# Kernel optimization log

Measured on AMD Instinct MI355X. Metric: run time of the kernel, lower is better.

## Reference

```python
import jax, jax.numpy as jnp
import numpy as np

B, C, H, W = 8, 512, 64, 64
HID = 4 * C  # MixFFN hidden = in_dim*4
FOCUS = 3.0


def _ln(x, g, b, eps=1e-5):
    m = x.mean(-1, keepdims=True)
    v = ((x - m) ** 2).mean(-1, keepdims=True)
    return (x - m) / jnp.sqrt(v + eps) * g + b


def setup_inputs() -> dict:
    key = jax.random.key(0)
    ks = jax.random.split(key, 12)
    init = lambda k, shape, fan: (jax.random.normal(k, shape, jnp.float32) / np.float32(np.sqrt(fan)))
    d = {}
    d['x'] = jax.random.normal(ks[0], (B, C, H, W), jnp.float32)
    # 1x1 conv weights stored as (Cout, Cin)
    d['Wq'] = init(ks[1], (C, C), C); d['bq'] = jnp.zeros((C,), jnp.float32)
    d['Wk'] = init(ks[2], (C, C), C); d['bk'] = jnp.zeros((C,), jnp.float32)
    d['Wv'] = init(ks[3], (C, C), C); d['bv'] = jnp.zeros((C,), jnp.float32)
    d['scale'] = jnp.zeros((1, 1, C), jnp.float32)  # nn.Parameter(torch.zeros)
    # MixFFN_skip params
    d['fc1_w'] = init(ks[4], (C, HID), C); d['fc1_b'] = jnp.zeros((HID,), jnp.float32)
    d['dw_w'] = init(ks[5], (HID, 1, 3, 3), 9); d['dw_b'] = jnp.zeros((HID,), jnp.float32)
    d['fc2_w'] = init(ks[6], (HID, C), HID); d['fc2_b'] = jnp.zeros((C,), jnp.float32)
    d['ln1_g'] = jnp.ones((HID,), jnp.float32); d['ln1_b'] = jnp.zeros((HID,), jnp.float32)
    d['lnm_g'] = jnp.ones((C,), jnp.float32); d['lnm_b'] = jnp.zeros((C,), jnp.float32)
    return d


def _forward(x, Wq, bq, Wk, bk, Wv, bv, scale, fc1_w, fc1_b, dw_w, dw_b, fc2_w, fc2_b, ln1_g, ln1_b, lnm_g, lnm_b):
    b, c, h, w = x.shape
    n = h * w
    # 1x1 convs (NCHW), then RAW reshape to (B, N, C) as in torch (no permute!)
    conv1 = lambda t, Wm, bm: jnp.einsum('bchw,oc->bohw', t, Wm) + bm[None, :, None, None]
    q = jax.nn.softmax(conv1(x, Wq, bq).reshape(b, n, c), axis=1)
    k = jax.nn.softmax(conv1(x, Wk, bk).reshape(b, n, c), axis=2)
    v = conv1(x, Wv, bv).reshape(b, n, c)
    q = jax.nn.relu(q) + 1e-6
    k = jax.nn.relu(k) + 1e-6
    sc = jax.nn.softplus(scale)
    q = q / sc
    k = k / sc
    q_norm = jnp.linalg.norm(q, axis=-1, keepdims=True)
    k_norm = jnp.linalg.norm(k, axis=-1, keepdims=True)
    q = q ** FOCUS  # focusing_factor <= 6 branch
    k = k ** FOCUS
    q = q / jnp.linalg.norm(q, axis=-1, keepdims=True) * q_norm
    k = k / jnp.linalg.norm(k, axis=-1, keepdims=True) * k_norm
    # num_heads == 1: (b h) n c == b n c
    z = 1.0 / (jnp.einsum('bic,bc->bi', q, k.sum(axis=1)) + 1e-6)
    kv = jnp.einsum('bjc,bjd->bcd', k, v)  # O(N) linear attention summary
    attn = jnp.einsum('bic,bcd,bi->bid', q, kv, z)
    shortcut = jnp.transpose(x, (0, 2, 3, 1)).reshape(b, n, c)  # proper rearrange b c h w -> b (h w) c
    enhanced = shortcut + attn
    # MixFFN_skip(norm_mlp(enhanced), h, w)
    t = _ln(enhanced, lnm_g, lnm_b)
    a = t @ fc1_w + fc1_b  # (B, N, HID)
    ai = jnp.transpose(a, (0, 2, 1)).reshape(b, HID, h, w)
    dw = jax.lax.conv_general_dilated(ai, dw_w, (1, 1), 'SAME',
                                      dimension_numbers=('NCHW', 'OIHW', 'NCHW'),
                                      feature_group_count=HID)
    dw = dw + dw_b[None, :, None, None]
    dw = jnp.transpose(dw.reshape(b, HID, n), (0, 2, 1))
    ax = jax.nn.gelu(_ln(dw + a, ln1_g, ln1_b), approximate=False)
    mlp_out = ax @ fc2_w + fc2_b
    out = enhanced + mlp_out
    return out.reshape(b, h, w, c)


def reference(x, Wq, bq, Wk, bk, Wv, bv, scale, fc1_w, fc1_b, dw_w, dw_b, fc2_w, fc2_b, ln1_g, ln1_b, lnm_g, lnm_b):
    return _forward(x, Wq, bq, Wk, bk, Wv, bv, scale, fc1_w, fc1_b, dw_w, dw_b, fc2_w, fc2_b, ln1_g, ln1_b, lnm_g, lnm_b)
```

## Files before the change

### kernel.cpp

```cpp
#include <hip/hip_runtime.h>
#include <hip/hip_bf16.h>

typedef __hip_bfloat16 bf16;
typedef __attribute__((ext_vector_type(8))) short bh8;
typedef __attribute__((ext_vector_type(4))) short bh4;
typedef __attribute__((ext_vector_type(4))) float f32x4;

#define CDIM 512
#define NDIM 4096
#define HIDD 2048
#define BATCH 8

__device__ __forceinline__ float bf2f(short s) {
    union { unsigned u; float f; } c; c.u = ((unsigned)(unsigned short)s) << 16; return c.f;
}
__device__ __forceinline__ short f2bf(float f) {
    union { __hip_bfloat16 h; short s; } c; c.h = __float2bfloat16(f); return c.s;
}
__device__ __forceinline__ float wsum(float v) {
#pragma unroll
    for (int o = 32; o; o >>= 1) v += __shfl_xor(v, o);
    return v;
}
__device__ __forceinline__ float wmax(float v) {
#pragma unroll
    for (int o = 32; o; o >>= 1) v = fmaxf(v, __shfl_xor(v, o));
    return v;
}

#define GLL(g, l) __builtin_amdgcn_global_load_lds( \
    (const __attribute__((address_space(1))) unsigned int*)(g), \
    (__attribute__((address_space(3))) unsigned int*)(l), 16, 0, 0)

enum { EP_QEXP = 0, EP_BF16_BROW = 1, EP_ATTN = 3, EP_BF16_BCOL = 4, EP_OUT = 5, EP_QKV = 6 };

template<int MODE, int TM, int MFAST>
__global__ __launch_bounds__(256)
void gemm_bt(const bf16* __restrict__ A, int lda, long sA,
             const bf16* __restrict__ Bt, int ldb, long sB,
             void* __restrict__ Cp, int ldc, long sC, int K,
             const float* __restrict__ bias,
             const void* __restrict__ aux1, long sAux1,
             const void* __restrict__ aux2, long sAux2)
{
    constexpr int MF = TM / 32;
    __shared__ __align__(16) bf16 As[TM * 64];
    __shared__ __align__(16) bf16 Bs[128 * 64];
    int bx, by, bz;
    {
        const int gx = gridDim.x, gy = gridDim.y;
        const int nwg = gx * gy * gridDim.z;
        int lid = blockIdx.x + gx * (blockIdx.y + gy * blockIdx.z);
        const int cpx = nwg >> 3;
        int swz = (lid & 7) * cpx + (lid >> 3);
        if constexpr (MFAST) {
            by = swz % gy; swz /= gy;
            bx = swz % gx;
            bz = swz / gx;
        } else {
            bx = swz % gx; swz /= gx;
            by = swz % gy;
            bz = swz / gy;
        }
    }
    const bf16* Ab = A + (long)bz * sA + (long)by * TM * lda;
    const bf16* Bb = Bt + (long)bz * sB + (long)bx * 128 * ldb;
    const int t = threadIdx.x, lane = t & 63, wid = t >> 6;
    const int wm = wid >> 1, wn = wid & 1, lg = lane >> 4, lr = lane & 15;

    f32x4 acc[MF][4];
#pragma unroll
    for (int m = 0; m < MF; ++m)
#pragma unroll
        for (int n = 0; n < 4; ++n) acc[m][n] = (f32x4){0.f, 0.f, 0.f, 0.f};

    for (int kt = 0; kt < K; kt += 64) {
#pragma unroll
        for (int i = 0; i < MF; ++i) {
            const int ch = i * 256 + t;
            const int row = ch >> 3;
            const int cs = (ch & 7) ^ (row & 7);
            GLL(Ab + (long)row * lda + kt + (cs << 3), (char*)As + i * 4096 + wid * 1024);
        }
#pragma unroll
        for (int i = 0; i < 4; ++i) {
            const int ch = i * 256 + t;
            const int row = ch >> 3;
            const int cs = (ch & 7) ^ (row & 7);
            GLL(Bb + (long)row * ldb + kt + (cs << 3), (char*)Bs + i * 4096 + wid * 1024);
        }
        __syncthreads();
#pragma unroll
        for (int kk = 0; kk < 2; ++kk) {
            bh8 af[MF], bfv[4];
#pragma unroll
            for (int m = 0; m < MF; ++m) {
                const int row = wm * (TM / 2) + m * 16 + lr;
                const int kc = (kk * 4 + lg) ^ (row & 7);
                af[m] = *(const bh8*)(As + row * 64 + kc * 8);
            }
#pragma unroll
            for (int n = 0; n < 4; ++n) {
                const int row = wn * 64 + n * 16 + lr;
                const int kc = (kk * 4 + lg) ^ (row & 7);
                bfv[n] = *(const bh8*)(Bs + row * 64 + kc * 8);
            }
#pragma unroll
            for (int m = 0; m < MF; ++m)
#pragma unroll
                for (int n = 0; n < 4; ++n)
                    acc[m][n] = __builtin_amdgcn_mfma_f32_16x16x32_bf16(af[m], bfv[n], acc[m][n], 0, 0, 0);
        }
        __syncthreads();
    }

    const int gr0 = by * TM + wm * (TM / 2);
    const int gc0 = bx * 128 + wn * 64;
#pragma unroll
    for (int m = 0; m < MF; ++m) {
#pragma unroll
        for (int n = 0; n < 4; ++n) {
            const int gc = gc0 + n * 16 + lr;
#pragma unroll
            for (int r = 0; r < 4; ++r) {
                const int gr = gr0 + m * 16 + lg * 4 + r;
                float v = acc[m][n][r];
                if constexpr (MODE == EP_QKV) {
                    const int which = gr >> 9, grl = gr & 511;
                    const float vb_ = v + bias[gr];
                    if (which == 0)
                        ((bf16*)Cp + (long)bz * sC)[(long)grl * ldc + gc] = __float2bfloat16(expf(vb_));
                    else if (which == 1)
                        ((bf16*)aux1 + (long)bz * sC)[(long)grl * ldc + gc] = __float2bfloat16(vb_);
                    else
                        ((bf16*)aux2 + (long)bz * sC)[(long)grl * ldc + gc] = __float2bfloat16(vb_);
                } else if constexpr (MODE == EP_QEXP) {
                    ((bf16*)Cp + (long)bz * sC)[(long)gr * ldc + gc] = __float2bfloat16(expf(v + bias[gr]));
                } else if constexpr (MODE == EP_BF16_BROW) {
                    ((bf16*)Cp + (long)bz * sC)[(long)gr * ldc + gc] = __float2bfloat16(v + bias[gr]);
                } else if constexpr (MODE == EP_ATTN) {
                    const bf16* xg = (const bf16*)aux1 + (long)bz * sAux1;
                    const float* zg = (const float*)aux2 + (long)bz * sAux2;
                    ((float*)Cp + (long)bz * sC)[(long)gr * ldc + gc] =
                        zg[gr] * v + bf2f(*(const short*)(xg + (long)gr * 512 + gc));
                } else if constexpr (MODE == EP_BF16_BCOL) {
                    ((bf16*)Cp + (long)bz * sC)[(long)gr * ldc + gc] = __float2bfloat16(v + bias[gc]);
                } else {
                    float* op = (float*)Cp;
                    const long idx = (long)gr * ldc + gc;
                    op[idx] = v + bias[gc] + ((const float*)aux1)[idx];
                }
            }
        }
    }
}

__global__ __launch_bounds__(256)
void gemm_tn_splitk(const bf16* __restrict__ A, int lda, long sA,
                    const bf16* __restrict__ B, int ldb, long sB,
                    bf16* __restrict__ part)
{
    __shared__ __align__(16) short As[64 * 128];
    __shared__ __align__(16) short Bs[64 * 128];
    int bx, by, bzl;
    {
        const int gx = gridDim.x, gy = gridDim.y;
        const int nwg = gx * gy * gridDim.z;
        int lid = blockIdx.x + gx * (blockIdx.y + gy * blockIdx.z);
        const int cpx = nwg >> 3;
        int swz = (lid & 7) * cpx + (lid >> 3);
        bx = swz % gx; swz /= gx;
        by = swz % gy;
        bzl = swz / gy;
    }
    const int bz = bzl >> 2, ks = bzl & 3;
    const bf16* Ab = A + (long)bz * sA + (long)ks * 1024 * lda + by * 128;
    const bf16* Bb = B + (long)bz * sB + (long)ks * 1024 * ldb + bx * 128;
    const int t = threadIdx.x, lane = t & 63, wid = t >> 6;
    const int wm = wid >> 1, wn = wid & 1, lg = lane >> 4, lr = lane & 15;

    f32x4 acc[4][4];
#pragma unroll
    for (int m = 0; m < 4; ++m)
#pragma unroll
        for (int n = 0; n < 4; ++n) acc[m][n] = (f32x4){0.f, 0.f, 0.f, 0.f};

    for (int kt = 0; kt < 1024; kt += 64) {
#pragma unroll
        for (int i = 0; i < 4; ++i) {
            const int ch = i * 256 + t;
            const int row = ch >> 4;
            const int cs = (ch & 15) ^ (((row >> 3) & 3) << 1);
            GLL(Ab + (long)(kt + row) * lda + (cs << 3), (char*)As + i * 4096 + wid * 1024);
            GLL(Bb + (long)(kt + row) * ldb + (cs << 3), (char*)Bs + i * 4096 + wid * 1024);
        }
        __syncthreads();
#pragma unroll
        for (int kk = 0; kk < 2; ++kk) {
            bh8 af[4], bfv[4];
#pragma unroll
            for (int m = 0; m < 4; ++m) {
                const int col = wm * 64 + m * 16 + lr;
#pragma unroll
                for (int u = 0; u < 8; ++u) {
                    const int row = kk * 32 + lg * 8 + u;
                    af[m][u] = As[row * 128 + (((col >> 3) ^ (((row >> 3) & 3) << 1)) << 3) + (col & 7)];
                }
            }
#pragma unroll
            for (int n = 0; n < 4; ++n) {
                const int col = wn * 64 + n * 16 + lr;
#pragma unroll
                for (int u = 0; u < 8; ++u) {
                    const int row = kk * 32 + lg * 8 + u;
                    bfv[n][u] = Bs[row * 128 + (((col >> 3) ^ (((row >> 3) & 3) << 1)) << 3) + (col & 7)];
                }
            }
#pragma unroll
            for (int m = 0; m < 4; ++m)
#pragma unroll
                for (int n = 0; n < 4; ++n)
                    acc[m][n] = __builtin_amdgcn_mfma_f32_16x16x32_bf16(af[m], bfv[n], acc[m][n], 0, 0, 0);
        }
        __syncthreads();
    }

    bf16* po = part + ((long)bzl << 18);
    const int gr0 = by * 128 + wm * 64;
    const int gc0 = bx * 128 + wn * 64;
#pragma unroll
    for (int m = 0; m < 4; ++m)
#pragma unroll
        for (int n = 0; n < 4; ++n) {
            const int gc = gc0 + n * 16 + lr;
#pragma unroll
            for (int r = 0; r < 4; ++r) {
                const int gr = gr0 + m * 16 + lg * 4 + r;
                po[(long)gr * 512 + gc] = __float2bfloat16(acc[m][n][r]);
            }
        }
}

__global__ __launch_bounds__(256)
void k_kvred(const bf16* __restrict__ part, bf16* __restrict__ kvt)
{
    const long e = ((long)blockIdx.x * 256 + threadIdx.x) * 8;
    const int b = (int)(e >> 18);
    const int off = (int)(e & 262143);
    float s[8] = {0.f, 0.f, 0.f, 0.f, 0.f, 0.f, 0.f, 0.f};
#pragma unroll
    for (int ks = 0; ks < 4; ++ks) {
        bh8 v = *(const bh8*)(part + (((long)(b * 4 + ks)) << 18) + off);
#pragma unroll
        for (int j = 0; j < 8; ++j) s[j] += bf2f(v[j]);
    }
    bh8 o;
#pragma unroll
    for (int j = 0; j < 8; ++j) o[j] = f2bf(s[j]);
    *(bh8*)(kvt + ((long)b << 18) + off) = o;
}

__global__ __launch_bounds__(256)
void k_transpose(const float* __restrict__ src, bf16* __restrict__ dst,
                 int Rd, int Cd, long sSrc, long sDst)
{
    __shared__ float tile[64][65];
    const float* s = src + (long)blockIdx.z * sSrc;
    bf16* d = dst + (long)blockIdx.z * sDst;
    const int r0 = blockIdx.x * 64, c0 = blockIdx.y * 64;
    const int t = threadIdx.x;
#pragma unroll 4
    for (int i = 0; i < 16; ++i) {
        int idx = i * 256 + t;
        int a = idx >> 6, b = idx & 63;
        tile[a][b] = s[(long)(c0 + a) * Rd + r0 + b];
    }
    __syncthreads();
#pragma unroll 4
    for (int i = 0; i < 16; ++i) {
        int idx = i * 256 + t;
        int a = idx >> 6, b = idx & 63;
        d[(long)(r0 + a) * Cd + c0 + b] = __float2bfloat16(tile[b][a]);
    }
}

__global__ void k_setup(const float* __restrict__ Wq, const float* __restrict__ Wk,
                        const float* __restrict__ Wv, bf16* __restrict__ oq,
                        bf16* __restrict__ ok, bf16* __restrict__ ov,
                        const float* __restrict__ scale, float* __restrict__ invsc,
                        const float* __restrict__ w, float* __restrict__ wT,
                        const float* __restrict__ bq, const float* __restrict__ bk,
                        const float* __restrict__ bv, float* __restrict__ bqkv) {
    int i = blockIdx.x * 256 + threadIdx.x;
    if (i < 262144) {
        oq[i] = __float2bfloat16(Wq[i]);
        ok[i] = __float2bfloat16(Wk[i]);
        ov[i] = __float2bfloat16(Wv[i]);
    }
    if (i < 512) invsc[i] = 1.0f / log1pf(expf(scale[i]));
    if (i < 1536) bqkv[i] = (i < 512 ? bq[i] : (i < 1024 ? bk[i - 512] : bv[i - 1024]));
    if (i < HIDD * 9) {
        int chn = i / 9, kk = i % 9;
        wT[kk * HIDD + chn] = w[i];
    }
}

__global__ void k_fill(float* o, int n, float v) {
    int i = blockIdx.x * 256 + threadIdx.x; if (i < n) o[i] = v;
}

__global__ __launch_bounds__(256)
void k_colsums(const bf16* __restrict__ qe, const bf16* __restrict__ kb,
               float* __restrict__ qpart, float* __restrict__ kpart) {
    const int xb = blockIdx.x;
    const int ic = blockIdx.y, b = blockIdx.z;
    const int j = (xb & 1) * 256 + threadIdx.x;
    const bf16* src = (xb < 2) ? qe : kb;
    const bf16* p = src + (long)b * (NDIM * CDIM) + (long)ic * 256 * CDIM + j;
    float s = 0.f;
    for (int i = 0; i < 256; ++i) s += bf2f(*(const short*)(p + (long)i * CDIM));
    ((xb < 2) ? qpart : kpart)[((long)b * 16 + ic) * CDIM + j] = s;
}

__global__ __launch_bounds__(256)
void k_red2(const float* __restrict__ qpart, float* __restrict__ qsum,
            const float* __restrict__ kpart, float* __restrict__ ksum) {
    const int idx = blockIdx.x * 256 + threadIdx.x;
    const int which = idx >> 12, r = idx & 4095;
    const int b = r >> 9, c = r & 511;
    const float* src = which ? kpart : qpart;
    float s = 0.f;
#pragma unroll
    for (int jc = 0; jc < 16; ++jc) s += src[((long)(b * 16 + jc)) * CDIM + c];
    (which ? ksum : qsum)[r] = s;
}

__global__ __launch_bounds__(256)
void k_qrow(const bf16* __restrict__ qe, const float* __restrict__ qsum,
            const float* __restrict__ invsc, bf16* __restrict__ qb,
            const float* __restrict__ ksum, float* __restrict__ z)
{
    const long row = (long)blockIdx.x * 4 + (threadIdx.x >> 6);
    const int lane = threadIdx.x & 63;
    const int b = (int)(row >> 12);
    bh8 ev = *(const bh8*)(qe + row * CDIM + lane * 8);
    const float* qs = qsum + b * CDIM + lane * 8;
    const float* is = invsc + lane * 8;
    f32x4 s0 = *(const f32x4*)qs, s1 = *(const f32x4*)(qs + 4);
    f32x4 i0 = *(const f32x4*)is, i1 = *(const f32x4*)(is + 4);
    float q[8];
#pragma unroll
    for (int k = 0; k < 4; ++k) {
        q[k]     = (bf2f(ev[k]) / s0[k] + 1e-6f) * i0[k];
        q[k + 4] = (bf2f(ev[k + 4]) / s1[k] + 1e-6f) * i1[k];
    }
    float s2 = 0.f, s6 = 0.f, q3[8];
#pragma unroll
    for (int k = 0; k < 8; ++k) { s2 += q[k] * q[k]; float c = q[k] * q[k] * q[k]; q3[k] = c; s6 += c * c; }
    s2 = wsum(s2); s6 = wsum(s6);
    const float sc = sqrtf(s2) / sqrtf(s6);
    bh8 o;
#pragma unroll
    for (int k = 0; k < 8; ++k) o[k] = f2bf(q3[k] * sc);
    *(bh8*)(qb + row * CDIM + lane * 8) = o;
    const float* ks = ksum + (long)b * CDIM + lane * 8;
    f32x4 k0 = *(const f32x4*)ks, k1 = *(const f32x4*)(ks + 4);
    float zd = 0.f;
#pragma unroll
    for (int j = 0; j < 4; ++j) { zd += bf2f(o[j]) * k0[j]; zd += bf2f(o[j + 4]) * k1[j]; }
    zd = wsum(zd);
    if (lane == 0) z[row] = 1.0f / (zd + 1e-6f);
}

__global__ __launch_bounds__(256)
void k_krow(bf16* __restrict__ kb, const float* __restrict__ invsc)
{
    const long row = (long)blockIdx.x * 4 + (threadIdx.x >> 6);
    const int lane = threadIdx.x & 63;
    bh8 v = *(const bh8*)(kb + row * CDIM + lane * 8);
    const float* is = invsc + lane * 8;
    f32x4 i0 = *(const f32x4*)is, i1 = *(const f32x4*)(is + 4);
    float xv[8];
#pragma unroll
    for (int k = 0; k < 8; ++k) xv[k] = bf2f(v[k]);
    float mx = -1e30f;
#pragma unroll
    for (int k = 0; k < 8; ++k) mx = fmaxf(mx, xv[k]);
    mx = wmax(mx);
    float e[8], se = 0.f;
#pragma unroll
    for (int k = 0; k < 8; ++k) { e[k] = expf(xv[k] - mx); se += e[k]; }
    se = wsum(se);
    const float inv = 1.0f / se;
    float q[8];
#pragma unroll
    for (int k = 0; k < 4; ++k) {
        q[k]     = (e[k] * inv + 1e-6f) * i0[k];
        q[k + 4] = (e[k + 4] * inv + 1e-6f) * i1[k];
    }
    float s2 = 0.f, s6 = 0.f, q3[8];
#pragma unroll
    for (int k = 0; k < 8; ++k) { s2 += q[k] * q[k]; float c = q[k] * q[k] * q[k]; q3[k] = c; s6 += c * c; }
    s2 = wsum(s2); s6 = wsum(s6);
    const float sc = sqrtf(s2) / sqrtf(s6);
    bh8 o;
#pragma unroll
    for (int k = 0; k < 8; ++k) o[k] = f2bf(q3[k] * sc);
    *(bh8*)(kb + row * CDIM + lane * 8) = o;
}

__global__ __launch_bounds__(256)
void k_ln512(const float* __restrict__ src, const float* __restrict__ g,
             const float* __restrict__ bta, bf16* __restrict__ dst)
{
    const long row = (long)blockIdx.x * 4 + (threadIdx.x >> 6);
    const int lane = threadIdx.x & 63;
    const float* p = src + row * CDIM + lane * 8;
    f32x4 a0 = *(const f32x4*)p, a1 = *(const f32x4*)(p + 4);
    float s = 0.f, ss = 0.f;
#pragma unroll
    for (int k = 0; k < 4; ++k) { s += a0[k] + a1[k]; ss += a0[k] * a0[k] + a1[k] * a1[k]; }
    s = wsum(s); ss = wsum(ss);
    const float mean = s * (1.0f / 512), var = ss * (1.0f / 512) - mean * mean;
    const float rstd = rsqrtf(var + 1e-5f);
    const float* gp = g + lane * 8;
    const float* bp = bta + lane * 8;
    f32x4 g0 = *(const f32x4*)gp, g1 = *(const f32x4*)(gp + 4);
    f32x4 b0 = *(const f32x4*)bp, b1 = *(const f32x4*)(bp + 4);
    bh8 o;
#pragma unroll
    for (int k = 0; k < 4; ++k) {
        o[k]     = f2bf((a0[k] - mean) * rstd * g0[k] + b0[k]);
        o[k + 4] = f2bf((a1[k] - mean) * rstd * g1[k] + b1[k]);
    }
    *(bh8*)(dst + row * CDIM + lane * 8) = o;
}

__global__ __launch_bounds__(256)
void k_dwlngelu4(const bf16* __restrict__ a, const float* __restrict__ dwwT,
                 const float* __restrict__ dwb, const float* __restrict__ g1,
                 const float* __restrict__ b1, bf16* __restrict__ ax)
{
    const long s0 = (long)blockIdx.x * 4;
    const int h = (int)((s0 >> 6) & 63);
    const int w0 = (int)(s0 & 63);
    const int ch = threadIdx.x * 8;

    float wgt[9][8];
#pragma unroll
    for (int kk = 0; kk < 9; ++kk) {
        f32x4 w0v = *(const f32x4*)(dwwT + kk * HIDD + ch);
        f32x4 w1v = *(const f32x4*)(dwwT + kk * HIDD + ch + 4);
#pragma unroll
        for (int j = 0; j < 4; ++j) { wgt[kk][j] = w0v[j]; wgt[kk][j + 4] = w1v[j]; }
    }
#pragma unroll
    for (int j = 0; j < 8; ++j) wgt[4][j] += 1.0f;

    float acc[4][8];
    {
        f32x4 d0 = *(const f32x4*)(dwb + ch), d1 = *(const f32x4*)(dwb + ch + 4);
#pragma unroll
        for (int ti = 0; ti < 4; ++ti)
#pragma unroll
            for (int j = 0; j < 4; ++j) { acc[ti][j] = d0[j]; acc[ti][j + 4] = d1[j]; }
    }

#pragma unroll
    for (int dy = -1; dy <= 1; ++dy) {
        const int hh = h + dy;
        if ((unsigned)hh >= 64u) continue;
#pragma unroll
        for (int c = -1; c <= 4; ++c) {
            const int ww = w0 + c;
            if ((unsigned)ww >= 64u) continue;
            bh8 v = *(const bh8*)(a + (s0 + (long)dy * 64 + c) * HIDD + ch);
            float f[8];
#pragma unroll
            for (int j = 0; j < 8; ++j) f[j] = bf2f(v[j]);
#pragma unroll
            for (int ti = 0; ti < 4; ++ti) {
                const int dx = c - ti;
                if (dx < -1 || dx > 1) continue;
                const int kk = (dy + 1) * 3 + (dx + 1);
#pragma unroll
                for (int j = 0; j < 8; ++j) acc[ti][j] += wgt[kk][j] * f[j];
            }
        }
    }

    float sv[4], qv[4];
#pragma unroll
    for (int ti = 0; ti < 4; ++ti) {
        float s = 0.f, q = 0.f;
#pragma unroll
        for (int j = 0; j < 8; ++j) { s += acc[ti][j]; q += acc[ti][j] * acc[ti][j]; }
        sv[ti] = wsum(s); qv[ti] = wsum(q);
    }
    __shared__ float red[4][4][2];
    const int wid = threadIdx.x >> 6, lane = threadIdx.x & 63;
    if (lane == 0)
#pragma unroll
        for (int ti = 0; ti < 4; ++ti) { red[wid][ti][0] = sv[ti]; red[wid][ti][1] = qv[ti]; }
    __syncthreads();

    f32x4 ga = *(const f32x4*)(g1 + ch), gb = *(const f32x4*)(g1 + ch + 4);
    f32x4 ba = *(const f32x4*)(b1 + ch), bb = *(const f32x4*)(b1 + ch + 4);
    float gg[8], bb8[8];
#pragma unroll
    for (int j = 0; j < 4; ++j) { gg[j] = ga[j]; gg[j + 4] = gb[j]; bb8[j] = ba[j]; bb8[j + 4] = bb[j]; }

#pragma unroll
    for (int ti = 0; ti < 4; ++ti) {
        const float s = red[0][ti][0] + red[1][ti][0] + red[2][ti][0] + red[3][ti][0];
        const float q = red[0][ti][1] + red[1][ti][1] + red[2][ti][1] + red[3][ti][1];
        const float mean = s * (1.0f / 2048), var = q * (1.0f / 2048) - mean * mean;
        const float rstd = rsqrtf(var + 1e-5f);
        bh8 o;
#pragma unroll
        for (int j = 0; j < 8; ++j) {
            float y = (acc[ti][j] - mean) * rstd * gg[j] + bb8[j];
            o[j] = f2bf(0.5f * y * (1.0f + erff(y * 0.70710678118654752f)));
        }
        *(bh8*)(ax + (s0 + ti) * HIDD + ch) = o;
    }
}

extern "C" void kernel_launch(void* const* d_in, const int* in_sizes, int n_in,
                              void* d_out, int out_size, void* d_ws, size_t ws_size,
                              hipStream_t stream) {
    const float* x     = (const float*)d_in[0];
    const float* Wq    = (const float*)d_in[1];
    const float* bq    = (const float*)d_in[2];
    const float* Wk    = (const float*)d_in[3];
    const float* bk    = (const float*)d_in[4];
    const float* Wv    = (const float*)d_in[5];
    const float* bv    = (const float*)d_in[6];
    const float* scale = (const float*)d_in[7];
    const float* fc1_w = (const float*)d_in[8];
    const float* fc1_b = (const float*)d_in[9];
    const float* dw_w  = (const float*)d_in[10];
    const float* dw_b  = (const float*)d_in[11];
    const float* fc2_w = (const float*)d_in[12];
    const float* fc2_b = (const float*)d_in[13];
    const float* ln1_g = (const float*)d_in[14];
    const float* ln1_b = (const float*)d_in[15];
    const float* lnm_g = (const float*)d_in[16];
    const float* lnm_b = (const float*)d_in[17];
    float* out = (float*)d_out;
    char* p = (char*)d_ws;

    bf16*  xbT   = (bf16*)(p + 0);
    bf16*  kb    = (bf16*)(p + 33554432);
    bf16*  vb    = (bf16*)(p + 67108864);
    bf16*  kvt   = (bf16*)(p + 100663296);
    bf16*  wqb   = (bf16*)(p + 104857600);
    bf16*  wkb   = (bf16*)(p + 105381888);
    bf16*  wvb   = (bf16*)(p + 105906176);
    bf16*  fc1wT = (bf16*)(p + 106430464);
    bf16*  fc2wT = (bf16*)(p + 108527616);
    float* invsc = (float*)(p + 110624768);
    float* dwwT  = (float*)(p + 110626816);
    float* bqkv  = (float*)(p + 110700544);
    float* qsum  = (float*)(p + 110757888);
    float* ksum  = (float*)(p + 110905344);
    float* zbuf  = (float*)(p + 110921728);
    const size_t REQUIRED = 111052800;
    float* qpart = (float*)kvt;
    float* kpart = (float*)((char*)kvt + 262144);
    bf16*  qe    = (bf16*)out;
    bf16*  kvpart= (bf16*)((char*)out + 33554432);
    bf16*  qb    = kb;
    bf16*  abuf  = (bf16*)(p + 0);
    bf16*  axbuf = (bf16*)(p + 33554432);
    bf16*  tbuf  = (bf16*)(p + 67108864);

    if (ws_size < REQUIRED) {
        k_fill<<<(out_size + 255) / 256, 256, 0, stream>>>(out, out_size, 100000.0f + (float)(ws_size >> 20));
        return;
    }

    const long NC = (long)NDIM * CDIM;

    k_setup<<<1024, 256, 0, stream>>>(Wq, Wk, Wv, wqb, wkb, wvb, scale, invsc,
                                      dw_w, dwwT, bq, bk, bv, bqkv);
    k_transpose<<<dim3(32, 8, 1), 256, 0, stream>>>(fc1_w, fc1wT, 2048, 512, 0, 0);
    k_transpose<<<dim3(8, 32, 1), 256, 0, stream>>>(fc2_w, fc2wT, 512, 2048, 0, 0);
    k_transpose<<<dim3(64, 8, BATCH), 256, 0, stream>>>(x, xbT, 4096, 512, NC, NC);

    gemm_bt<EP_QKV, 128, 1><<<dim3(32, 12, 8), 256, 0, stream>>>(
        wqb, 512, 0, xbT, 512, NC, qe, 4096, NC, 512, bqkv, kb, 0, vb, 0);

    k_krow<<<8192, 256, 0, stream>>>(kb, invsc);
    k_colsums<<<dim3(4, 16, 8), 256, 0, stream>>>(qe, kb, qpart, kpart);
    k_red2<<<32, 256, 0, stream>>>(qpart, qsum, kpart, ksum);

    gemm_tn_splitk<<<dim3(4, 4, 32), 256, 0, stream>>>(vb, 512, NC, kb, 512, NC, kvpart);
    k_kvred<<<1024, 256, 0, stream>>>(kvpart, kvt);

    k_qrow<<<8192, 256, 0, stream>>>(qe, qsum, invsc, qb, ksum, zbuf);

    gemm_bt<EP_ATTN, 128, 0><<<dim3(4, 32, 8), 256, 0, stream>>>(
        qb, 512, NC, kvt, 512, 262144, out, 512, NC, 512, nullptr, xbT, NC, zbuf, 4096);

    k_ln512<<<8192, 256, 0, stream>>>(out, lnm_g, lnm_b, tbuf);
    for (int q4 = 0; q4 < 4; ++q4) {
        float* outq = out + (long)q4 * 8192 * CDIM;
        bf16* tq = tbuf + (long)q4 * 8192 * CDIM;
        gemm_bt<EP_BF16_BCOL, 128, 0><<<dim3(16, 64, 1), 256, 0, stream>>>(
            tq, 512, 0, fc1wT, 512, 0, abuf, 2048, 0, 512, fc1_b, nullptr, 0, nullptr, 0);
        k_dwlngelu4<<<2048, 256, 0, stream>>>(abuf, dwwT, dw_b, ln1_g, ln1_b, axbuf);
        gemm_bt<EP_OUT, 64, 0><<<dim3(4, 128, 1), 256, 0, stream>>>(
            axbuf, 2048, 0, fc2wT, 2048, 0, outq, 512, 0, 2048, fc2_b, outq, 0, nullptr, 0);
    }
}
```

Measured before the change: 631.9 us.

## Stage GEMM epilogues through LDS for coalesced stores and merge small kernels

The QKV and fc1 GEMM epilogues and the split-K kv GEMM now write bf16 results into a swizzled shared-memory tile, then issue 16-byte coalesced global stores instead of scattered 2-byte stores. The three transpose launches are merged into one kernel, and the kv reduction is folded into the q-row kernel to cut launch count. Both the QKV epilogue and k_krow also switch expf to the faster __expf. The trade-offs are an extra LDS round trip with a barrier in each epilogue and slightly lower exp precision.

```diff
diff --git a/kernel.cpp b/kernel.cpp
--- a/kernel.cpp
+++ b/kernel.cpp
@@ -3,7 +3,6 @@
 
 typedef __hip_bfloat16 bf16;
 typedef __attribute__((ext_vector_type(8))) short bh8;
-typedef __attribute__((ext_vector_type(4))) short bh4;
 typedef __attribute__((ext_vector_type(4))) float f32x4;
 
 #define CDIM 512
@@ -32,7 +31,7 @@
     (const __attribute__((address_space(1))) unsigned int*)(g), \
     (__attribute__((address_space(3))) unsigned int*)(l), 16, 0, 0)
 
-enum { EP_QEXP = 0, EP_BF16_BROW = 1, EP_ATTN = 3, EP_BF16_BCOL = 4, EP_OUT = 5, EP_QKV = 6 };
+enum { EP_BF16_BROW = 1, EP_ATTN = 3, EP_BF16_BCOL = 4, EP_OUT = 5, EP_QKV = 6 };
 
 template<int MODE, int TM, int MFAST>
 __global__ __launch_bounds__(256)
@@ -44,8 +43,9 @@
              const void* __restrict__ aux2, long sAux2)
 {
     constexpr int MF = TM / 32;
-    __shared__ __align__(16) bf16 As[TM * 64];
-    __shared__ __align__(16) bf16 Bs[128 * 64];
+    __shared__ __align__(16) bf16 smem[TM * 64 + 128 * 64];
+    bf16* As = smem;
+    bf16* Bs = smem + TM * 64;
     int bx, by, bz;
     {
         const int gx = gridDim.x, gy = gridDim.y;
@@ -114,6 +114,44 @@
         __syncthreads();
     }
 
+    if constexpr (TM == 128 && (MODE == EP_QKV || MODE == EP_BF16_BCOL)) {
+        bf16* Cs = smem;
+        bf16* dstb;
+        bool doexp = false;
+        if constexpr (MODE == EP_QKV) {
+            const int which = by >> 2;
+            if (which == 0) { dstb = (bf16*)Cp; doexp = true; }
+            else if (which == 1) dstb = (bf16*)aux1;
+            else dstb = (bf16*)aux2;
+            dstb += (long)bz * sC + (long)((by & 3) * 128) * ldc;
+        } else {
+            dstb = (bf16*)Cp + (long)bz * sC + (long)by * 128 * ldc;
+        }
+#pragma unroll
+        for (int m = 0; m < MF; ++m)
+#pragma unroll
+            for (int n = 0; n < 4; ++n)
+#pragma unroll
+                for (int r = 0; r < 4; ++r) {
+                    const int row = wm * 64 + m * 16 + lg * 4 + r;
+                    const int col = wn * 64 + n * 16 + lr;
+                    float v = acc[m][n][r];
+                    if constexpr (MODE == EP_QKV) v += bias[by * 128 + row];
+                    else v += bias[bx * 128 + col];
+                    if (doexp) v = __expf(v);
+                    Cs[row * 128 + (col ^ (((row >> 2) & 3) << 4))] = __float2bfloat16(v);
+                }
+        __syncthreads();
+#pragma unroll
+        for (int it = 0; it < 8; ++it) {
+            const int id = it * 256 + t;
+            const int row = id >> 4, colc = (id & 15) << 3;
+            bh8 v = *(const bh8*)(Cs + row * 128 + (colc ^ (((row >> 2) & 3) << 4)));
+            *(bh8*)(dstb + (long)row * ldc + bx * 128 + colc) = v;
+        }
+        return;
+    }
+
     const int gr0 = by * TM + wm * (TM / 2);
     const int gc0 = bx * 128 + wn * 64;
 #pragma unroll
@@ -125,27 +163,14 @@
             for (int r = 0; r < 4; ++r) {
                 const int gr = gr0 + m * 16 + lg * 4 + r;
                 float v = acc[m][n][r];
-                if constexpr (MODE == EP_QKV) {
-                    const int which = gr >> 9, grl = gr & 511;
-                    const float vb_ = v + bias[gr];
-                    if (which == 0)
-                        ((bf16*)Cp + (long)bz * sC)[(long)grl * ldc + gc] = __float2bfloat16(expf(vb_));
-                    else if (which == 1)
-                        ((bf16*)aux1 + (long)bz * sC)[(long)grl * ldc + gc] = __float2bfloat16(vb_);
-                    else
-                        ((bf16*)aux2 + (long)bz * sC)[(long)grl * ldc + gc] = __float2bfloat16(vb_);
-                } else if constexpr (MODE == EP_QEXP) {
-                    ((bf16*)Cp + (long)bz * sC)[(long)gr * ldc + gc] = __float2bfloat16(expf(v + bias[gr]));
-                } else if constexpr (MODE == EP_BF16_BROW) {
+                if constexpr (MODE == EP_BF16_BROW) {
                     ((bf16*)Cp + (long)bz * sC)[(long)gr * ldc + gc] = __float2bfloat16(v + bias[gr]);
                 } else if constexpr (MODE == EP_ATTN) {
                     const bf16* xg = (const bf16*)aux1 + (long)bz * sAux1;
                     const float* zg = (const float*)aux2 + (long)bz * sAux2;
                     ((float*)Cp + (long)bz * sC)[(long)gr * ldc + gc] =
                         zg[gr] * v + bf2f(*(const short*)(xg + (long)gr * 512 + gc));
-                } else if constexpr (MODE == EP_BF16_BCOL) {
-                    ((bf16*)Cp + (long)bz * sC)[(long)gr * ldc + gc] = __float2bfloat16(v + bias[gc]);
-                } else {
+                } else if constexpr (MODE == EP_OUT) {
                     float* op = (float*)Cp;
                     const long idx = (long)gr * ldc + gc;
                     op[idx] = v + bias[gc] + ((const float*)aux1)[idx];
@@ -160,8 +185,9 @@
                     const bf16* __restrict__ B, int ldb, long sB,
                     bf16* __restrict__ part)
 {
-    __shared__ __align__(16) short As[64 * 128];
-    __shared__ __align__(16) short Bs[64 * 128];
+    __shared__ __align__(16) short smem[2 * 64 * 128];
+    short* As = smem;
+    short* Bs = smem + 64 * 128;
     int bx, by, bzl;
     {
         const int gx = gridDim.x, gy = gridDim.y;
@@ -225,49 +251,49 @@
         __syncthreads();
     }
 
-    bf16* po = part + ((long)bzl << 18);
-    const int gr0 = by * 128 + wm * 64;
-    const int gc0 = bx * 128 + wn * 64;
+    bf16* Cs = (bf16*)smem;
+    bf16* dstb = part + ((long)bzl << 18) + (long)by * 128 * 512;
 #pragma unroll
     for (int m = 0; m < 4; ++m)
 #pragma unroll
-        for (int n = 0; n < 4; ++n) {
-            const int gc = gc0 + n * 16 + lr;
+        for (int n = 0; n < 4; ++n)
 #pragma unroll
             for (int r = 0; r < 4; ++r) {
-                const int gr = gr0 + m * 16 + lg * 4 + r;
-                po[(long)gr * 512 + gc] = __float2bfloat16(acc[m][n][r]);
+                const int row = wm * 64 + m * 16 + lg * 4 + r;
+                const int col = wn * 64 + n * 16 + lr;
+                Cs[row * 128 + (col ^ (((row >> 2) & 3) << 4))] = __float2bfloat16(acc[m][n][r]);
             }
-        }
-}
-
-__global__ __launch_bounds__(256)
-void k_kvred(const bf16* __restrict__ part, bf16* __restrict__ kvt)
-{
-    const long e = ((long)blockIdx.x * 256 + threadIdx.x) * 8;
-    const int b = (int)(e >> 18);
-    const int off = (int)(e & 262143);
-    float s[8] = {0.f, 0.f, 0.f, 0.f, 0.f, 0.f, 0.f, 0.f};
-#pragma unroll
-    for (int ks = 0; ks < 4; ++ks) {
-        bh8 v = *(const bh8*)(part + (((long)(b * 4 + ks)) << 18) + off);
-#pragma unroll
-        for (int j = 0; j < 8; ++j) s[j] += bf2f(v[j]);
-    }
-    bh8 o;
-#pragma unroll
-    for (int j = 0; j < 8; ++j) o[j] = f2bf(s[j]);
-    *(bh8*)(kvt + ((long)b << 18) + off) = o;
-}
-
-__global__ __launch_bounds__(256)
-void k_transpose(const float* __restrict__ src, bf16* __restrict__ dst,
-                 int Rd, int Cd, long sSrc, long sDst)
+    __syncthreads();
+#pragma unroll
+    for (int it = 0; it < 8; ++it) {
+        const int id = it * 256 + t;
+        const int row = id >> 4, colc = (id & 15) << 3;
+        bh8 v = *(const bh8*)(Cs + row * 128 + (colc ^ (((row >> 2) & 3) << 4)));
+        *(bh8*)(dstb + (long)row * 512 + bx * 128 + colc) = v;
+    }
+}
+
+__global__ __launch_bounds__(256)
+void k_transpose3(const float* __restrict__ fc1w, bf16* __restrict__ fc1wT,
+                  const float* __restrict__ fc2w, bf16* __restrict__ fc2wT,
+                  const float* __restrict__ x, bf16* __restrict__ xbT)
 {
     __shared__ float tile[64][65];
-    const float* s = src + (long)blockIdx.z * sSrc;
-    bf16* d = dst + (long)blockIdx.z * sDst;
-    const int r0 = blockIdx.x * 64, c0 = blockIdx.y * 64;
+    const int bid = blockIdx.x;
+    const float* s; bf16* d; int Rd, Cd, bx, by;
+    if (bid < 256) {
+        s = fc1w; d = fc1wT; Rd = 2048; Cd = 512; bx = bid & 31; by = bid >> 5;
+    } else if (bid < 512) {
+        const int i = bid - 256;
+        s = fc2w; d = fc2wT; Rd = 512; Cd = 2048; bx = i & 7; by = i >> 3;
+    } else {
+        const int i = bid - 512;
+        const int bz = i >> 9, j = i & 511;
+        bx = j & 63; by = j >> 6;
+        const long NC = (long)NDIM * CDIM;
+        s = x + (long)bz * NC; d = xbT + (long)bz * NC; Rd = 4096; Cd = 512;
+    }
+    const int r0 = bx * 64, c0 = by * 64;
     const int t = threadIdx.x;
 #pragma unroll 4
     for (int i = 0; i < 16; ++i) {
@@ -336,11 +362,29 @@
 }
 
 __global__ __launch_bounds__(256)
-void k_qrow(const bf16* __restrict__ qe, const float* __restrict__ qsum,
-            const float* __restrict__ invsc, bf16* __restrict__ qb,
-            const float* __restrict__ ksum, float* __restrict__ z)
+void k_kvqrow(const bf16* __restrict__ part, bf16* __restrict__ kvt,
+              const bf16* __restrict__ qe, const float* __restrict__ qsum,
+              const float* __restrict__ invsc, bf16* __restrict__ qb,
+              const float* __restrict__ ksum, float* __restrict__ z)
 {
-    const long row = (long)blockIdx.x * 4 + (threadIdx.x >> 6);
+    if (blockIdx.x < 1024) {
+        const long e = ((long)blockIdx.x * 256 + threadIdx.x) * 8;
+        const int b = (int)(e >> 18);
+        const int off = (int)(e & 262143);
+        float s[8] = {0.f, 0.f, 0.f, 0.f, 0.f, 0.f, 0.f, 0.f};
+#pragma unroll
+        for (int ks = 0; ks < 4; ++ks) {
+            bh8 v = *(const bh8*)(part + (((long)(b * 4 + ks)) << 18) + off);
+#pragma unroll
+            for (int j = 0; j < 8; ++j) s[j] += bf2f(v[j]);
+        }
+        bh8 o;
+#pragma unroll
+        for (int j = 0; j < 8; ++j) o[j] = f2bf(s[j]);
+        *(bh8*)(kvt + ((long)b << 18) + off) = o;
+        return;
+    }
+    const long row = (long)(blockIdx.x - 1024) * 4 + (threadIdx.x >> 6);
     const int lane = threadIdx.x & 63;
     const int b = (int)(row >> 12);
     bh8 ev = *(const bh8*)(qe + row * CDIM + lane * 8);
@@ -389,7 +433,7 @@
     mx = wmax(mx);
     float e[8], se = 0.f;
 #pragma unroll
-    for (int k = 0; k < 8; ++k) { e[k] = expf(xv[k] - mx); se += e[k]; }
+    for (int k = 0; k < 8; ++k) { e[k] = __expf(xv[k] - mx); se += e[k]; }
     se = wsum(se);
     const float inv = 1.0f / se;
     float q[8];
@@ -584,9 +628,7 @@
 
     k_setup<<<1024, 256, 0, stream>>>(Wq, Wk, Wv, wqb, wkb, wvb, scale, invsc,
                                       dw_w, dwwT, bq, bk, bv, bqkv);
-    k_transpose<<<dim3(32, 8, 1), 256, 0, stream>>>(fc1_w, fc1wT, 2048, 512, 0, 0);
-    k_transpose<<<dim3(8, 32, 1), 256, 0, stream>>>(fc2_w, fc2wT, 512, 2048, 0, 0);
-    k_transpose<<<dim3(64, 8, BATCH), 256, 0, stream>>>(x, xbT, 4096, 512, NC, NC);
+    k_transpose3<<<4608, 256, 0, stream>>>(fc1_w, fc1wT, fc2_w, fc2wT, x, xbT);
 
     gemm_bt<EP_QKV, 128, 1><<<dim3(32, 12, 8), 256, 0, stream>>>(
         wqb, 512, 0, xbT, 512, NC, qe, 4096, NC, 512, bqkv, kb, 0, vb, 0);
@@ -596,9 +638,7 @@
     k_red2<<<32, 256, 0, stream>>>(qpart, qsum, kpart, ksum);
 
     gemm_tn_splitk<<<dim3(4, 4, 32), 256, 0, stream>>>(vb, 512, NC, kb, 512, NC, kvpart);
-    k_kvred<<<1024, 256, 0, stream>>>(kvpart, kvt);
-
-    k_qrow<<<8192, 256, 0, stream>>>(qe, qsum, invsc, qb, ksum, zbuf);
+    k_kvqrow<<<9216, 256, 0, stream>>>(kvpart, kvt, qe, qsum, invsc, qb, ksum, zbuf);
 
     gemm_bt<EP_ATTN, 128, 0><<<dim3(4, 32, 8), 256, 0, stream>>>(
         qb, 512, NC, kvt, 512, 262144, out, 512, NC, 512, nullptr, xbT, NC, zbuf, 4096);
```

New measurement: 613.2 us. 1.03x faster.
